# Performance work log

Measured on AMD Instinct MI355X. Metric: run time of the kernel, lower is better.

## Reference

```python
import jax, jax.numpy as jnp
import numpy as np

N, E, D, R = 8192, 131072, 128, 32
SIZES = (3, 5, 7)  # per-degree component counts (2l+1)
LN_EPS = 1e-5


def setup_inputs() -> dict:
    key = jax.random.key(0)
    ks = jax.random.split(key, 20)
    rn = lambda k, shape, s=1.0: jax.random.normal(k, shape, jnp.float32) * s
    inp = {
        'X0': rn(ks[0], (N, SIZES[0], D)),
        'X1': rn(ks[1], (N, SIZES[1], D)),
        'X2': rn(ks[2], (N, SIZES[2], D)),
        't_ij': rn(ks[3], (E, D)),
        'r0': rn(ks[4], (E, SIZES[0])),
        'r1': rn(ks[5], (E, SIZES[1])),
        'r2': rn(ks[6], (E, SIZES[2])),
        'edge_index': jax.random.randint(ks[7], (2, E), 0, N, dtype=jnp.int32),
        # params
        'W_vq': rn(ks[8], (D, R), D ** -0.5),
        'W_vk0': rn(ks[9], (D, R), D ** -0.5),
        'W_vk1': rn(ks[10], (D, R), D ** -0.5),
        'W_vk2': rn(ks[11], (D, R), D ** -0.5),
        'ln_g': jnp.ones((R,), jnp.float32),
        'ln_b': jnp.zeros((R,), jnp.float32),
        'W_w': rn(ks[12], (R, D), R ** -0.5),
        'b_w': jnp.zeros((D,), jnp.float32),
        'W_t1': rn(ks[13], (D, D), D ** -0.5),
        'b_t1': jnp.zeros((D,), jnp.float32),
        'W_t2': rn(ks[14], (D, D), D ** -0.5),
        'b_t2': jnp.zeros((D,), jnp.float32),
    }
    return inp


def _vec_rej(x, r):
    # x: [E, L, R], r: [E, L]; dot over component dim (L), keepdim, subtract projection
    r = r[..., None]
    dot = jnp.sum(x * r, axis=1, keepdims=True)  # [E, 1, R]
    return x - dot * r


def reference(X0, X1, X2, t_ij, r0, r1, r2, edge_index,
              W_vq, W_vk0, W_vk1, W_vk2, ln_g, ln_b, W_w, b_w,
              W_t1, b_t1, W_t2, b_t2):
    n_j, n_i = edge_index[0], edge_index[1]
    X_ls = jnp.concatenate([X0, X1, X2], axis=1)                 # [N, 15, D]
    eq_i = jnp.einsum('nld,dr->nlr', X_ls, W_vq)[n_i]            # [E, 15, R]
    ek = jnp.concatenate([
        jnp.einsum('nld,dr->nlr', X0, W_vk0),
        jnp.einsum('nld,dr->nlr', X1, W_vk1),
        jnp.einsum('nld,dr->nlr', X2, W_vk2)], axis=1)
    ek_j = ek[n_j]                                               # [E, 15, R]
    # per-degree vector rejection (vec_rej=True)
    qs, ksl, off = [], [], 0
    for r in (r0, r1, r2):
        s = r.shape[1]
        qs.append(_vec_rej(eq_i[:, off:off + s], r))
        ksl.append(_vec_rej(ek_j[:, off:off + s], -r))
        off += s
    eq_i = jnp.concatenate(qs, axis=1)
    ek_j = jnp.concatenate(ksl, axis=1)
    w_ij = jnp.sum(eq_i * ek_j, axis=1)                          # [E, R]
    # mlp_w = LayerNorm + Linear
    mu = jnp.mean(w_ij, axis=-1, keepdims=True)
    var = jnp.var(w_ij, axis=-1, keepdims=True)
    wn = (w_ij - mu) * jax.lax.rsqrt(var + LN_EPS) * ln_g + ln_b
    dw = wn @ W_w + b_w                                          # [E, D]
    # mlp_t = Linear -> silu -> Linear, then outer activation
    t = jax.nn.silu(t_ij @ W_t1 + b_t1) @ W_t2 + b_t2            # [E, D]
    return dw * jax.nn.silu(t)
```

## Files before the change

kernel.cpp:

```cpp
#include <hip/hip_runtime.h>
#include <hip/hip_bf16.h>

#define N_NODES 8192
#define N_EDGES 131072
#define LN_EPS  1e-5f

typedef __attribute__((ext_vector_type(8))) short bf16x8;
typedef __attribute__((ext_vector_type(4))) float f32x4;

__device__ __forceinline__ float silu_f(float x) {
    return x / (1.0f + __expf(-x));
}

__device__ __forceinline__ unsigned short f2bf(float x) {
    union { float f; unsigned int u; } v; v.f = x;
    unsigned int r = v.u + 0x7FFFu + ((v.u >> 16) & 1u);
    return (unsigned short)(r >> 16);
}
__device__ __forceinline__ float bf2f(unsigned short u) {
    union { float f; unsigned int x; } v; v.x = ((unsigned int)u) << 16;
    return v.f;
}
__device__ __forceinline__ unsigned int pk2(float a, float b) {
    return (unsigned int)f2bf(a) | ((unsigned int)f2bf(b) << 16);
}
__device__ __forceinline__ f32x4 mfma16(bf16x8 a, bf16x8 b, f32x4 c) {
    return __builtin_amdgcn_mfma_f32_16x16x32_bf16(a, b, c, 0, 0, 0);
}

__global__ __launch_bounds__(256) void prep_kernel(
    const float* __restrict__ W_w, const float* __restrict__ W_t1,
    const float* __restrict__ W_t2, const float* __restrict__ Wvq,
    const float* __restrict__ Wvk0, const float* __restrict__ Wvk1,
    const float* __restrict__ Wvk2,
    unsigned short* __restrict__ Wtw, unsigned short* __restrict__ Wt1b,
    unsigned short* __restrict__ Wt2b, unsigned short* __restrict__ Wqt,
    unsigned short* __restrict__ Wk0t, unsigned short* __restrict__ Wk1t,
    unsigned short* __restrict__ Wk2t)
{
    int i = blockIdx.x * 256 + threadIdx.x;
    if (i < 16384) {
        int n = i >> 7, k = i & 127;
        Wt1b[i] = f2bf(W_t1[k * 128 + n]);
        Wt2b[i] = f2bf(W_t2[k * 128 + n]);
    }
    if (i < 4096) {
        { int n = i >> 5, k = i & 31; Wtw[i] = f2bf(W_w[k * 128 + n]); }
        int r = i >> 7, d = i & 127;
        Wqt[i]  = f2bf(Wvq [d * 32 + r]);
        Wk0t[i] = f2bf(Wvk0[d * 32 + r]);
        Wk1t[i] = f2bf(Wvk1[d * 32 + r]);
        Wk2t[i] = f2bf(Wvk2[d * 32 + r]);
    }
}

template<int S, int LOFF>
__device__ __forceinline__ void proj_body(
    const float* __restrict__ X, const unsigned short* __restrict__ Wqt,
    const unsigned short* __restrict__ Wkt,
    unsigned short* __restrict__ eq, unsigned short* __restrict__ ek,
    int row0, unsigned short* Xl)
{
    const int tid = threadIdx.x;
    #pragma unroll
    for (int i = 0; i < 4; ++i) {
        int c   = tid + i * 256;
        int row = c >> 4;
        int ke  = (c & 15) * 8;
        const float* src = &X[(size_t)(row0 + row) * 128 + ke];
        float4 a0 = *(const float4*)src;
        float4 a1 = *(const float4*)(src + 4);
        uint4 p;
        p.x = pk2(a0.x, a0.y); p.y = pk2(a0.z, a0.w);
        p.z = pk2(a1.x, a1.y); p.w = pk2(a1.z, a1.w);
        *(uint4*)((char*)Xl + ((row * 256 + ke * 2) ^ ((row & 7) << 4))) = p;
    }
    __syncthreads();

    const int lane  = tid & 63;
    const int wv    = tid >> 6;
    const int l15   = lane & 15;
    const int lk    = lane >> 4;
    const int strip = wv * 16;
    const int xrow_l = strip + l15;

    f32x4 qa[2], ka[2];
    #pragma unroll
    for (int h = 0; h < 2; ++h) {
        qa[h] = (f32x4){0.f, 0.f, 0.f, 0.f};
        ka[h] = (f32x4){0.f, 0.f, 0.f, 0.f};
    }

    #pragma unroll
    for (int kt = 0; kt < 4; ++kt) {
        bf16x8 x = *(const bf16x8*)((const char*)Xl +
            ((xrow_l * 256 + kt * 64 + lk * 16) ^ ((xrow_l & 7) << 4)));
        #pragma unroll
        for (int h = 0; h < 2; ++h) {
            bf16x8 wq = *(const bf16x8*)&Wqt[(h * 16 + l15) * 128 + kt * 32 + lk * 8];
            bf16x8 wk = *(const bf16x8*)&Wkt[(h * 16 + l15) * 128 + kt * 32 + lk * 8];
            qa[h] = mfma16(wq, x, qa[h]);
            ka[h] = mfma16(wk, x, ka[h]);
        }
    }

    const int xrow = row0 + strip + l15;
    const int n = xrow / S;
    const int l = xrow % S + LOFF;
    const size_t base = (size_t)n * 480 + (size_t)l * 32;
    #pragma unroll
    for (int h = 0; h < 2; ++h) {
        int rb = h * 16 + lk * 4;
        ushort4 pq, pk_;
        pq.x = f2bf(qa[h][0]); pq.y = f2bf(qa[h][1]);
        pq.z = f2bf(qa[h][2]); pq.w = f2bf(qa[h][3]);
        pk_.x = f2bf(ka[h][0]); pk_.y = f2bf(ka[h][1]);
        pk_.z = f2bf(ka[h][2]); pk_.w = f2bf(ka[h][3]);
        *(ushort4*)&eq[base + rb] = pq;
        *(ushort4*)&ek[base + rb] = pk_;
    }
}

__global__ __launch_bounds__(256) void proj_kernel(
    const float* __restrict__ X0, const float* __restrict__ X1,
    const float* __restrict__ X2,
    const unsigned short* __restrict__ Wqt,
    const unsigned short* __restrict__ Wk0t,
    const unsigned short* __restrict__ Wk1t,
    const unsigned short* __restrict__ Wk2t,
    unsigned short* __restrict__ eq, unsigned short* __restrict__ ek)
{
    __shared__ __align__(16) unsigned short Xl[64 * 128];
    const int b = blockIdx.x;
    if (b < 384)
        proj_body<3, 0>(X0, Wqt, Wk0t, eq, ek, b * 64, Xl);
    else if (b < 1024)
        proj_body<5, 3>(X1, Wqt, Wk1t, eq, ek, (b - 384) * 64, Xl);
    else
        proj_body<7, 8>(X2, Wqt, Wk2t, eq, ek, (b - 1024) * 64, Xl);
}

__global__ __launch_bounds__(256) void wn_kernel(
    const unsigned short* __restrict__ eq, const unsigned short* __restrict__ ek,
    const float* __restrict__ r0, const float* __restrict__ r1,
    const float* __restrict__ r2, const int* __restrict__ eidx,
    const float* __restrict__ ln_g, const float* __restrict__ ln_b,
    unsigned short* __restrict__ wn)
{
    const int tid = threadIdx.x;
    const int r   = tid & 31;
    const int e   = blockIdx.x * 8 + (tid >> 5);
    const float g  = ln_g[r];
    const float bb = ln_b[r];
    const int nj = eidx[e];
    const int ni = eidx[N_EDGES + e];

    float q[15], k[15], rv[15];
    const unsigned short* qp = eq + (size_t)ni * 480 + r;
    const unsigned short* kp = ek + (size_t)nj * 480 + r;
    #pragma unroll
    for (int l = 0; l < 15; ++l) { q[l] = bf2f(qp[l * 32]); k[l] = bf2f(kp[l * 32]); }
    #pragma unroll
    for (int c = 0; c < 3; ++c) rv[c]     = r0[e * 3 + c];
    #pragma unroll
    for (int c = 0; c < 5; ++c) rv[3 + c] = r1[e * 5 + c];
    #pragma unroll
    for (int c = 0; c < 7; ++c) rv[8 + c] = r2[e * 7 + c];

    float dq, dk;
    dq = q[0]*rv[0] + q[1]*rv[1] + q[2]*rv[2];
    dk = k[0]*rv[0] + k[1]*rv[1] + k[2]*rv[2];
    #pragma unroll
    for (int l = 0; l < 3; ++l) { q[l] -= dq * rv[l]; k[l] -= dk * rv[l]; }
    dq = 0.f; dk = 0.f;
    #pragma unroll
    for (int l = 3; l < 8; ++l) { dq += q[l]*rv[l]; dk += k[l]*rv[l]; }
    #pragma unroll
    for (int l = 3; l < 8; ++l) { q[l] -= dq * rv[l]; k[l] -= dk * rv[l]; }
    dq = 0.f; dk = 0.f;
    #pragma unroll
    for (int l = 8; l < 15; ++l) { dq += q[l]*rv[l]; dk += k[l]*rv[l]; }
    #pragma unroll
    for (int l = 8; l < 15; ++l) { q[l] -= dq * rv[l]; k[l] -= dk * rv[l]; }

    float w = 0.f;
    #pragma unroll
    for (int l = 0; l < 15; ++l) w = fmaf(q[l], k[l], w);

    float s = w, s2 = w * w;
    s += __shfl_xor(s, 1);  s2 += __shfl_xor(s2, 1);
    s += __shfl_xor(s, 2);  s2 += __shfl_xor(s2, 2);
    s += __shfl_xor(s, 4);  s2 += __shfl_xor(s2, 4);
    s += __shfl_xor(s, 8);  s2 += __shfl_xor(s2, 8);
    s += __shfl_xor(s, 16); s2 += __shfl_xor(s2, 16);
    const float mu  = s * (1.f / 32.f);
    const float var = s2 * (1.f / 32.f) - mu * mu;
    const float wnv = (w - mu) * rsqrtf(var + LN_EPS) * g + bb;
    wn[(size_t)e * 32 + r] = f2bf(wnv);
}

__global__ __launch_bounds__(256) void edge_kernel(
    const float* __restrict__ t_ij,
    const unsigned short* __restrict__ wn,
    const unsigned short* __restrict__ Wtw, const float* __restrict__ b_w,
    const unsigned short* __restrict__ Wt1, const float* __restrict__ b_t1,
    const unsigned short* __restrict__ Wt2, const float* __restrict__ b_t2,
    float* __restrict__ out)
{
    __shared__ __align__(16) unsigned short At[64 * 128];
    __shared__ __align__(16) unsigned short Ht[64 * 128];

    const int tid  = threadIdx.x;
    const int tile = blockIdx.x * 64;

    #pragma unroll
    for (int i = 0; i < 4; ++i) {
        int c   = tid + i * 256;
        int row = c >> 4;
        int ke  = (c & 15) * 8;
        const float* src = &t_ij[(size_t)(tile + row) * 128 + ke];
        float4 a0 = *(const float4*)src;
        float4 a1 = *(const float4*)(src + 4);
        uint4 p;
        p.x = pk2(a0.x, a0.y); p.y = pk2(a0.z, a0.w);
        p.z = pk2(a1.x, a1.y); p.w = pk2(a1.z, a1.w);
        *(uint4*)((char*)At + ((row * 256 + ke * 2) ^ ((row & 7) << 4))) = p;
    }

    const int lane = tid & 63;
    const int wv   = tid >> 6;
    const int wc   = wv * 32;
    const int l15  = lane & 15;
    const int lk   = lane >> 4;

    bf16x8 wwf[2];
    #pragma unroll
    for (int ct = 0; ct < 2; ++ct)
        wwf[ct] = *(const bf16x8*)&Wtw[(wc + ct * 16 + l15) * 32 + lk * 8];

    f32x4 dac[4][2];
    #pragma unroll
    for (int rt = 0; rt < 4; ++rt) {
        bf16x8 a = *(const bf16x8*)&wn[(size_t)(tile + rt * 16 + l15) * 32 + lk * 8];
        dac[rt][0] = mfma16(a, wwf[0], (f32x4){0.f, 0.f, 0.f, 0.f});
        dac[rt][1] = mfma16(a, wwf[1], (f32x4){0.f, 0.f, 0.f, 0.f});
    }

    __syncthreads();

    bf16x8 w1f[4][2];
    #pragma unroll
    for (int kt = 0; kt < 4; ++kt)
        #pragma unroll
        for (int ct = 0; ct < 2; ++ct)
            w1f[kt][ct] = *(const bf16x8*)
                &Wt1[(size_t)(wc + ct * 16 + l15) * 128 + kt * 32 + lk * 8];

    f32x4 tac[4][2];
    #pragma unroll
    for (int rt = 0; rt < 4; ++rt)
        #pragma unroll
        for (int ct = 0; ct < 2; ++ct)
            tac[rt][ct] = (f32x4){0.f, 0.f, 0.f, 0.f};

    #pragma unroll
    for (int kt = 0; kt < 4; ++kt) {
        #pragma unroll
        for (int rt = 0; rt < 4; ++rt) {
            int row = rt * 16 + l15;
            bf16x8 a = *(const bf16x8*)((const char*)At +
                ((row * 256 + kt * 64 + lk * 16) ^ ((row & 7) << 4)));
            tac[rt][0] = mfma16(a, w1f[kt][0], tac[rt][0]);
            tac[rt][1] = mfma16(a, w1f[kt][1], tac[rt][1]);
        }
    }

    {
        float bt1v0 = b_t1[wc + l15];
        float bt1v1 = b_t1[wc + 16 + l15];
        #pragma unroll
        for (int rt = 0; rt < 4; ++rt)
            #pragma unroll
            for (int ct = 0; ct < 2; ++ct) {
                float bb  = ct ? bt1v1 : bt1v0;
                int   col = wc + ct * 16 + l15;
                #pragma unroll
                for (int r = 0; r < 4; ++r) {
                    int row = rt * 16 + lk * 4 + r;
                    float hv = silu_f(tac[rt][ct][r] + bb);
                    *(unsigned short*)((char*)Ht +
                        ((row * 256 + col * 2) ^ ((row & 7) << 4))) = f2bf(hv);
                }
            }
    }
    __syncthreads();

    bf16x8 w2f[4][2];
    #pragma unroll
    for (int kt = 0; kt < 4; ++kt)
        #pragma unroll
        for (int ct = 0; ct < 2; ++ct)
            w2f[kt][ct] = *(const bf16x8*)
                &Wt2[(size_t)(wc + ct * 16 + l15) * 128 + kt * 32 + lk * 8];

    f32x4 oac[4][2];
    #pragma unroll
    for (int rt = 0; rt < 4; ++rt)
        #pragma unroll
        for (int ct = 0; ct < 2; ++ct)
            oac[rt][ct] = (f32x4){0.f, 0.f, 0.f, 0.f};

    #pragma unroll
    for (int kt = 0; kt < 4; ++kt) {
        #pragma unroll
        for (int rt = 0; rt < 4; ++rt) {
            int row = rt * 16 + l15;
            bf16x8 a = *(const bf16x8*)((const char*)Ht +
                ((row * 256 + kt * 64 + lk * 16) ^ ((row & 7) << 4)));
            oac[rt][0] = mfma16(a, w2f[kt][0], oac[rt][0]);
            oac[rt][1] = mfma16(a, w2f[kt][1], oac[rt][1]);
        }
    }

    {
        float bw0 = b_w[wc + l15],  bw1 = b_w[wc + 16 + l15];
        float b20 = b_t2[wc + l15], b21 = b_t2[wc + 16 + l15];
        #pragma unroll
        for (int rt = 0; rt < 4; ++rt)
            #pragma unroll
            for (int ct = 0; ct < 2; ++ct) {
                float bwv = ct ? bw1 : bw0;
                float b2v = ct ? b21 : b20;
                int   col = wc + ct * 16 + l15;
                #pragma unroll
                for (int r = 0; r < 4; ++r) {
                    int row = rt * 16 + lk * 4 + r;
                    float dwv = dac[rt][ct][r] + bwv;
                    float tv  = silu_f(oac[rt][ct][r] + b2v);
                    out[(size_t)(tile + row) * 128 + col] = dwv * tv;
                }
            }
    }
}

extern "C" void kernel_launch(void* const* d_in, const int* in_sizes, int n_in,
                              void* d_out, int out_size, void* d_ws, size_t ws_size,
                              hipStream_t stream) {
    (void)in_sizes; (void)n_in; (void)out_size; (void)ws_size;
    const float* X0   = (const float*)d_in[0];
    const float* X1   = (const float*)d_in[1];
    const float* X2   = (const float*)d_in[2];
    const float* t_ij = (const float*)d_in[3];
    const float* r0   = (const float*)d_in[4];
    const float* r1   = (const float*)d_in[5];
    const float* r2   = (const float*)d_in[6];
    const int*   eidx = (const int*)d_in[7];
    const float* Wvq  = (const float*)d_in[8];
    const float* Wvk0 = (const float*)d_in[9];
    const float* Wvk1 = (const float*)d_in[10];
    const float* Wvk2 = (const float*)d_in[11];
    const float* ln_g = (const float*)d_in[12];
    const float* ln_b = (const float*)d_in[13];
    const float* W_w  = (const float*)d_in[14];
    const float* b_w  = (const float*)d_in[15];
    const float* W_t1 = (const float*)d_in[16];
    const float* b_t1 = (const float*)d_in[17];
    const float* W_t2 = (const float*)d_in[18];
    const float* b_t2 = (const float*)d_in[19];
    float* out = (float*)d_out;

    unsigned short* eq   = (unsigned short*)d_ws;
    unsigned short* ek   = eq  + (size_t)N_NODES * 480;
    unsigned short* wn   = ek  + (size_t)N_NODES * 480;
    unsigned short* Wtw  = wn  + (size_t)N_EDGES * 32;
    unsigned short* Wt1b = Wtw  + 4096;
    unsigned short* Wt2b = Wt1b + 16384;
    unsigned short* Wqt  = Wt2b + 16384;
    unsigned short* Wk0t = Wqt  + 4096;
    unsigned short* Wk1t = Wk0t + 4096;
    unsigned short* Wk2t = Wk1t + 4096;

    prep_kernel<<<64, 256, 0, stream>>>(W_w, W_t1, W_t2, Wvq, Wvk0, Wvk1, Wvk2,
                                        Wtw, Wt1b, Wt2b, Wqt, Wk0t, Wk1t, Wk2t);
    proj_kernel<<<1920, 256, 0, stream>>>(X0, X1, X2, Wqt, Wk0t, Wk1t, Wk2t,
                                          eq, ek);
    wn_kernel<<<N_EDGES / 8, 256, 0, stream>>>(eq, ek, r0, r1, r2, eidx,
                                               ln_g, ln_b, wn);
    edge_kernel<<<N_EDGES / 64, 256, 0, stream>>>(t_ij, wn, Wtw, b_w,
                                                  Wt1b, b_t1, Wt2b, b_t2, out);
}
```

Baseline: 113.0 us.

## Give each wave its own edge rows and drop block-wide LDS staging

The edge kernel now gives each wavefront 32 private edge rows and computes all 128 output columns. It loads the t_ij fragments straight into registers and keeps the hidden activations in a per-wave LDS slice, which removes the block-wide __syncthreads barriers. The projection kernel likewise loads X fragments directly into registers instead of staging them through shared memory. bf16 packing now uses the hardware float2-to-bfloat162 conversion. In exchange, weight fragments are reloaded per column tile from global/L2, register pressure rises, and blocks cover 128 edges instead of 64.

```diff
diff --git a/kernel.cpp b/kernel.cpp
--- a/kernel.cpp
+++ b/kernel.cpp
@@ -22,7 +22,16 @@
     return v.f;
 }
 __device__ __forceinline__ unsigned int pk2(float a, float b) {
-    return (unsigned int)f2bf(a) | ((unsigned int)f2bf(b) << 16);
+    float2 t; t.x = a; t.y = b;
+    union { __hip_bfloat162 h; unsigned int u; } v;
+    v.h = __float22bfloat162_rn(t);
+    return v.u;
+}
+__device__ __forceinline__ bf16x8 pack8(float4 u, float4 v) {
+    union { bf16x8 b; unsigned int w[4]; } o;
+    o.w[0] = pk2(u.x, u.y); o.w[1] = pk2(u.z, u.w);
+    o.w[2] = pk2(v.x, v.y); o.w[3] = pk2(v.z, v.w);
+    return o.b;
 }
 __device__ __forceinline__ f32x4 mfma16(bf16x8 a, bf16x8 b, f32x4 c) {
     return __builtin_amdgcn_mfma_f32_16x16x32_bf16(a, b, c, 0, 0, 0);
@@ -59,30 +68,21 @@
     const float* __restrict__ X, const unsigned short* __restrict__ Wqt,
     const unsigned short* __restrict__ Wkt,
     unsigned short* __restrict__ eq, unsigned short* __restrict__ ek,
-    int row0, unsigned short* Xl)
-{
-    const int tid = threadIdx.x;
-    #pragma unroll
-    for (int i = 0; i < 4; ++i) {
-        int c   = tid + i * 256;
-        int row = c >> 4;
-        int ke  = (c & 15) * 8;
-        const float* src = &X[(size_t)(row0 + row) * 128 + ke];
-        float4 a0 = *(const float4*)src;
-        float4 a1 = *(const float4*)(src + 4);
-        uint4 p;
-        p.x = pk2(a0.x, a0.y); p.y = pk2(a0.z, a0.w);
-        p.z = pk2(a1.x, a1.y); p.w = pk2(a1.z, a1.w);
-        *(uint4*)((char*)Xl + ((row * 256 + ke * 2) ^ ((row & 7) << 4))) = p;
-    }
-    __syncthreads();
-
-    const int lane  = tid & 63;
-    const int wv    = tid >> 6;
-    const int l15   = lane & 15;
-    const int lk    = lane >> 4;
-    const int strip = wv * 16;
-    const int xrow_l = strip + l15;
+    int row0)
+{
+    const int tid  = threadIdx.x;
+    const int lane = tid & 63;
+    const int wv   = tid >> 6;
+    const int l15  = lane & 15;
+    const int lk   = lane >> 4;
+    const int xrow = row0 + wv * 16 + l15;
+
+    bf16x8 xf[4];
+    #pragma unroll
+    for (int kt = 0; kt < 4; ++kt) {
+        const float* p = X + (size_t)xrow * 128 + kt * 32 + lk * 8;
+        xf[kt] = pack8(*(const float4*)p, *(const float4*)(p + 4));
+    }
 
     f32x4 qa[2], ka[2];
     #pragma unroll
@@ -90,34 +90,28 @@
         qa[h] = (f32x4){0.f, 0.f, 0.f, 0.f};
         ka[h] = (f32x4){0.f, 0.f, 0.f, 0.f};
     }
-
     #pragma unroll
     for (int kt = 0; kt < 4; ++kt) {
-        bf16x8 x = *(const bf16x8*)((const char*)Xl +
-            ((xrow_l * 256 + kt * 64 + lk * 16) ^ ((xrow_l & 7) << 4)));
         #pragma unroll
         for (int h = 0; h < 2; ++h) {
             bf16x8 wq = *(const bf16x8*)&Wqt[(h * 16 + l15) * 128 + kt * 32 + lk * 8];
             bf16x8 wk = *(const bf16x8*)&Wkt[(h * 16 + l15) * 128 + kt * 32 + lk * 8];
-            qa[h] = mfma16(wq, x, qa[h]);
-            ka[h] = mfma16(wk, x, ka[h]);
-        }
-    }
-
-    const int xrow = row0 + strip + l15;
+            qa[h] = mfma16(wq, xf[kt], qa[h]);
+            ka[h] = mfma16(wk, xf[kt], ka[h]);
+        }
+    }
+
     const int n = xrow / S;
     const int l = xrow % S + LOFF;
     const size_t base = (size_t)n * 480 + (size_t)l * 32;
     #pragma unroll
     for (int h = 0; h < 2; ++h) {
         int rb = h * 16 + lk * 4;
-        ushort4 pq, pk_;
-        pq.x = f2bf(qa[h][0]); pq.y = f2bf(qa[h][1]);
-        pq.z = f2bf(qa[h][2]); pq.w = f2bf(qa[h][3]);
-        pk_.x = f2bf(ka[h][0]); pk_.y = f2bf(ka[h][1]);
-        pk_.z = f2bf(ka[h][2]); pk_.w = f2bf(ka[h][3]);
-        *(ushort4*)&eq[base + rb] = pq;
-        *(ushort4*)&ek[base + rb] = pk_;
+        union { ushort4 s; unsigned int u[2]; } pq, pk_;
+        pq.u[0]  = pk2(qa[h][0], qa[h][1]); pq.u[1]  = pk2(qa[h][2], qa[h][3]);
+        pk_.u[0] = pk2(ka[h][0], ka[h][1]); pk_.u[1] = pk2(ka[h][2], ka[h][3]);
+        *(ushort4*)&eq[base + rb] = pq.s;
+        *(ushort4*)&ek[base + rb] = pk_.s;
     }
 }
 
@@ -130,14 +124,13 @@
     const unsigned short* __restrict__ Wk2t,
     unsigned short* __restrict__ eq, unsigned short* __restrict__ ek)
 {
-    __shared__ __align__(16) unsigned short Xl[64 * 128];
     const int b = blockIdx.x;
     if (b < 384)
-        proj_body<3, 0>(X0, Wqt, Wk0t, eq, ek, b * 64, Xl);
+        proj_body<3, 0>(X0, Wqt, Wk0t, eq, ek, b * 64);
     else if (b < 1024)
-        proj_body<5, 3>(X1, Wqt, Wk1t, eq, ek, (b - 384) * 64, Xl);
+        proj_body<5, 3>(X1, Wqt, Wk1t, eq, ek, (b - 384) * 64);
     else
-        proj_body<7, 8>(X2, Wqt, Wk2t, eq, ek, (b - 1024) * 64, Xl);
+        proj_body<7, 8>(X2, Wqt, Wk2t, eq, ek, (b - 1024) * 64);
 }
 
 __global__ __launch_bounds__(256) void wn_kernel(
@@ -207,139 +200,97 @@
     const unsigned short* __restrict__ Wt2, const float* __restrict__ b_t2,
     float* __restrict__ out)
 {
-    __shared__ __align__(16) unsigned short At[64 * 128];
-    __shared__ __align__(16) unsigned short Ht[64 * 128];
+    __shared__ __align__(16) unsigned short Hp[4][32 * 128];
 
     const int tid  = threadIdx.x;
-    const int tile = blockIdx.x * 64;
-
-    #pragma unroll
-    for (int i = 0; i < 4; ++i) {
-        int c   = tid + i * 256;
-        int row = c >> 4;
-        int ke  = (c & 15) * 8;
-        const float* src = &t_ij[(size_t)(tile + row) * 128 + ke];
-        float4 a0 = *(const float4*)src;
-        float4 a1 = *(const float4*)(src + 4);
-        uint4 p;
-        p.x = pk2(a0.x, a0.y); p.y = pk2(a0.z, a0.w);
-        p.z = pk2(a1.x, a1.y); p.w = pk2(a1.z, a1.w);
-        *(uint4*)((char*)At + ((row * 256 + ke * 2) ^ ((row & 7) << 4))) = p;
-    }
-
     const int lane = tid & 63;
     const int wv   = tid >> 6;
-    const int wc   = wv * 32;
     const int l15  = lane & 15;
     const int lk   = lane >> 4;
-
-    bf16x8 wwf[2];
-    #pragma unroll
-    for (int ct = 0; ct < 2; ++ct)
-        wwf[ct] = *(const bf16x8*)&Wtw[(wc + ct * 16 + l15) * 32 + lk * 8];
-
-    f32x4 dac[4][2];
-    #pragma unroll
-    for (int rt = 0; rt < 4; ++rt) {
-        bf16x8 a = *(const bf16x8*)&wn[(size_t)(tile + rt * 16 + l15) * 32 + lk * 8];
-        dac[rt][0] = mfma16(a, wwf[0], (f32x4){0.f, 0.f, 0.f, 0.f});
-        dac[rt][1] = mfma16(a, wwf[1], (f32x4){0.f, 0.f, 0.f, 0.f});
-    }
-
-    __syncthreads();
-
-    bf16x8 w1f[4][2];
+    const int tile = (blockIdx.x * 4 + wv) * 32;
+    char* hp = (char*)&Hp[wv][0];
+
+    bf16x8 a1[4][2];
     #pragma unroll
     for (int kt = 0; kt < 4; ++kt)
         #pragma unroll
-        for (int ct = 0; ct < 2; ++ct)
-            w1f[kt][ct] = *(const bf16x8*)
-                &Wt1[(size_t)(wc + ct * 16 + l15) * 128 + kt * 32 + lk * 8];
-
-    f32x4 tac[4][2];
-    #pragma unroll
-    for (int rt = 0; rt < 4; ++rt)
-        #pragma unroll
-        for (int ct = 0; ct < 2; ++ct)
-            tac[rt][ct] = (f32x4){0.f, 0.f, 0.f, 0.f};
-
-    #pragma unroll
-    for (int kt = 0; kt < 4; ++kt) {
-        #pragma unroll
-        for (int rt = 0; rt < 4; ++rt) {
-            int row = rt * 16 + l15;
-            bf16x8 a = *(const bf16x8*)((const char*)At +
-                ((row * 256 + kt * 64 + lk * 16) ^ ((row & 7) << 4)));
-            tac[rt][0] = mfma16(a, w1f[kt][0], tac[rt][0]);
-            tac[rt][1] = mfma16(a, w1f[kt][1], tac[rt][1]);
-        }
-    }
-
-    {
-        float bt1v0 = b_t1[wc + l15];
-        float bt1v1 = b_t1[wc + 16 + l15];
-        #pragma unroll
-        for (int rt = 0; rt < 4; ++rt)
-            #pragma unroll
-            for (int ct = 0; ct < 2; ++ct) {
-                float bb  = ct ? bt1v1 : bt1v0;
-                int   col = wc + ct * 16 + l15;
-                #pragma unroll
-                for (int r = 0; r < 4; ++r) {
-                    int row = rt * 16 + lk * 4 + r;
-                    float hv = silu_f(tac[rt][ct][r] + bb);
-                    *(unsigned short*)((char*)Ht +
-                        ((row * 256 + col * 2) ^ ((row & 7) << 4))) = f2bf(hv);
-                }
-            }
-    }
-    __syncthreads();
-
-    bf16x8 w2f[4][2];
+        for (int rt = 0; rt < 2; ++rt) {
+            const float* p = t_ij + (size_t)(tile + rt * 16 + l15) * 128
+                           + kt * 32 + lk * 8;
+            a1[kt][rt] = pack8(*(const float4*)p, *(const float4*)(p + 4));
+        }
+
+    bf16x8 wnf[2];
+    #pragma unroll
+    for (int rt = 0; rt < 2; ++rt)
+        wnf[rt] = *(const bf16x8*)&wn[(size_t)(tile + rt * 16 + l15) * 32 + lk * 8];
+
+    #pragma unroll
+    for (int ct = 0; ct < 8; ++ct) {
+        bf16x8 w1f[4];
+        #pragma unroll
+        for (int kt = 0; kt < 4; ++kt)
+            w1f[kt] = *(const bf16x8*)&Wt1[(size_t)(ct * 16 + l15) * 128
+                                           + kt * 32 + lk * 8];
+        f32x4 ac0 = (f32x4){0.f, 0.f, 0.f, 0.f};
+        f32x4 ac1 = (f32x4){0.f, 0.f, 0.f, 0.f};
+        #pragma unroll
+        for (int kt = 0; kt < 4; ++kt) {
+            ac0 = mfma16(a1[kt][0], w1f[kt], ac0);
+            ac1 = mfma16(a1[kt][1], w1f[kt], ac1);
+        }
+        const float bb = b_t1[ct * 16 + l15];
+        const int   n  = ct * 16 + l15;
+        #pragma unroll
+        for (int r = 0; r < 4; ++r) {
+            int m0 = lk * 4 + r;
+            int m1 = 16 + lk * 4 + r;
+            *(unsigned short*)(hp + (((m0 * 128 + n) * 2) ^ ((m0 & 7) << 4)))
+                = f2bf(silu_f(ac0[r] + bb));
+            *(unsigned short*)(hp + (((m1 * 128 + n) * 2) ^ ((m1 & 7) << 4)))
+                = f2bf(silu_f(ac1[r] + bb));
+        }
+    }
+
+    bf16x8 a2[4][2];
     #pragma unroll
     for (int kt = 0; kt < 4; ++kt)
         #pragma unroll
-        for (int ct = 0; ct < 2; ++ct)
-            w2f[kt][ct] = *(const bf16x8*)
-                &Wt2[(size_t)(wc + ct * 16 + l15) * 128 + kt * 32 + lk * 8];
-
-    f32x4 oac[4][2];
-    #pragma unroll
-    for (int rt = 0; rt < 4; ++rt)
-        #pragma unroll
-        for (int ct = 0; ct < 2; ++ct)
-            oac[rt][ct] = (f32x4){0.f, 0.f, 0.f, 0.f};
-
-    #pragma unroll
-    for (int kt = 0; kt < 4; ++kt) {
-        #pragma unroll
-        for (int rt = 0; rt < 4; ++rt) {
-            int row = rt * 16 + l15;
-            bf16x8 a = *(const bf16x8*)((const char*)Ht +
-                ((row * 256 + kt * 64 + lk * 16) ^ ((row & 7) << 4)));
-            oac[rt][0] = mfma16(a, w2f[kt][0], oac[rt][0]);
-            oac[rt][1] = mfma16(a, w2f[kt][1], oac[rt][1]);
-        }
-    }
-
-    {
-        float bw0 = b_w[wc + l15],  bw1 = b_w[wc + 16 + l15];
-        float b20 = b_t2[wc + l15], b21 = b_t2[wc + 16 + l15];
-        #pragma unroll
-        for (int rt = 0; rt < 4; ++rt)
-            #pragma unroll
-            for (int ct = 0; ct < 2; ++ct) {
-                float bwv = ct ? bw1 : bw0;
-                float b2v = ct ? b21 : b20;
-                int   col = wc + ct * 16 + l15;
-                #pragma unroll
-                for (int r = 0; r < 4; ++r) {
-                    int row = rt * 16 + lk * 4 + r;
-                    float dwv = dac[rt][ct][r] + bwv;
-                    float tv  = silu_f(oac[rt][ct][r] + b2v);
-                    out[(size_t)(tile + row) * 128 + col] = dwv * tv;
-                }
-            }
+        for (int rt = 0; rt < 2; ++rt) {
+            int m2 = rt * 16 + l15;
+            a2[kt][rt] = *(const bf16x8*)(hp +
+                (((m2 * 128 + kt * 32 + lk * 8) * 2) ^ ((m2 & 7) << 4)));
+        }
+
+    #pragma unroll
+    for (int ct = 0; ct < 8; ++ct) {
+        bf16x8 w2f[4];
+        #pragma unroll
+        for (int kt = 0; kt < 4; ++kt)
+            w2f[kt] = *(const bf16x8*)&Wt2[(size_t)(ct * 16 + l15) * 128
+                                           + kt * 32 + lk * 8];
+        bf16x8 wwf = *(const bf16x8*)&Wtw[(ct * 16 + l15) * 32 + lk * 8];
+
+        f32x4 o0 = (f32x4){0.f, 0.f, 0.f, 0.f};
+        f32x4 o1 = (f32x4){0.f, 0.f, 0.f, 0.f};
+        #pragma unroll
+        for (int kt = 0; kt < 4; ++kt) {
+            o0 = mfma16(a2[kt][0], w2f[kt], o0);
+            o1 = mfma16(a2[kt][1], w2f[kt], o1);
+        }
+        f32x4 d0 = mfma16(wnf[0], wwf, (f32x4){0.f, 0.f, 0.f, 0.f});
+        f32x4 d1 = mfma16(wnf[1], wwf, (f32x4){0.f, 0.f, 0.f, 0.f});
+
+        const float bwv = b_w[ct * 16 + l15];
+        const float b2v = b_t2[ct * 16 + l15];
+        const int   n   = ct * 16 + l15;
+        #pragma unroll
+        for (int r = 0; r < 4; ++r) {
+            out[(size_t)(tile + lk * 4 + r) * 128 + n]
+                = (d0[r] + bwv) * silu_f(o0[r] + b2v);
+            out[(size_t)(tile + 16 + lk * 4 + r) * 128 + n]
+                = (d1[r] + bwv) * silu_f(o1[r] + b2v);
+        }
     }
 }
 
@@ -386,6 +337,6 @@
                                           eq, ek);
     wn_kernel<<<N_EDGES / 8, 256, 0, stream>>>(eq, ek, r0, r1, r2, eidx,
                                                ln_g, ln_b, wn);
-    edge_kernel<<<N_EDGES / 64, 256, 0, stream>>>(t_ij, wn, Wtw, b_w,
-                                                  Wt1b, b_t1, Wt2b, b_t2, out);
-}
+    edge_kernel<<<N_EDGES / 128, 256, 0, stream>>>(t_ij, wn, Wtw, b_w,
+                                                   Wt1b, b_t1, Wt2b, b_t2, out);
+}
```

Measured after the change: 114.5 us. About the same (+1.3%).
